# Kernel tuning notes

Measured on AMD Instinct MI355X. Metric: run time of the kernel, lower is better.

Reference implementation:

```python
import jax, jax.numpy as jnp
import numpy as np

N, E, IN, H1, H2 = 100000, 3200000, 128, 64, 64


def setup_inputs() -> dict:
    key = jax.random.key(0)
    ks = jax.random.split(key, 6)
    return {
        "edge_index": jax.random.randint(ks[0], (2, E), 0, N),
        "edge_weight": jax.random.uniform(ks[1], (E,), jnp.float32),
        "emb": jax.random.normal(ks[2], (N, IN), jnp.float32) * 0.05,  # xavier-initialized node embeddings
        "W1": jax.random.normal(ks[3], (IN, H1), jnp.float32) / np.sqrt(IN),
        "b1": jnp.zeros((H1,), jnp.float32),
        "W2": jax.random.normal(ks[4], (H1, H2), jnp.float32) / np.sqrt(H1),
        "b2": jnp.zeros((H2,), jnp.float32),
    }


def _digcn_conv(x, edge_index, edge_weight, W, b):
    # DIGCNConv: dense transform, then weighted sparse neighborhood sum-aggregation.
    x = x @ W                                              # [N, d_out]
    msg = edge_weight[:, None] * x[edge_index[0]]          # gather sources -> [E, d_out]
    out = jax.ops.segment_sum(msg, edge_index[1], num_segments=x.shape[0])  # scatter-add to targets
    return out + b


def reference(edge_index, edge_weight, emb, W1, b1, W2, b2):
    h = jax.nn.relu(_digcn_conv(emb, edge_index, edge_weight, W1, b1))
    # F.dropout with training=False is identity (inference mode)
    return _digcn_conv(h, edge_index, edge_weight, W2, b2)
```

## Files before the change

kernel.cpp:

```cpp
#include <hip/hip_runtime.h>
#include <hip/hip_bf16.h>

#define NNODES 100000
#define DIN 128
#define DH 64
#define SRCMASK 0x1FFFF
#define BSH2 8
#define BN2 256
#define NBUCK2 ((NNODES + BN2 - 1) >> BSH2)
#define NCAP 9088
#define EPB 8192
#define MAXBLK 512
#define OVFCAP 4096

typedef short s16x8 __attribute__((ext_vector_type(8)));
typedef float f32x4 __attribute__((ext_vector_type(4)));

static __device__ __forceinline__ short f2bf(float f) {
  __hip_bfloat16 h = __float2bfloat16(f);
  return *reinterpret_cast<short*>(&h);
}
static __device__ __forceinline__ float bf2f(short s) {
  return __uint_as_float(((unsigned)(unsigned short)s) << 16);
}


__global__ __launch_bounds__(256, 4) void gemm1_mfma(
    const float* __restrict__ emb, const float* __restrict__ W1,
    __hip_bfloat16* __restrict__ x1, int N) {
  __shared__ short Bhi[4 * 4 * 64 * 8];
  __shared__ short Blo[4 * 4 * 64 * 8];
  int tid = threadIdx.x;

  for (int idx = tid; idx < 8192; idx += 256) {
    int i = idx & 7, ln = (idx >> 3) & 63, ct = (idx >> 9) & 3, kc = idx >> 11;
    int k = kc * 32 + (ln >> 4) * 8 + i;
    int col = ct * 16 + (ln & 15);
    float w = W1[k * DH + col];
    short h = f2bf(w);
    Bhi[idx] = h;
    Blo[idx] = f2bf(w - bf2f(h));
  }
  __syncthreads();

  int lane = tid & 63, wv = tid >> 6;
  int r0 = (blockIdx.x * 8 + wv * 2) * 16;
  if (r0 >= N) return;

  const int rA = lane & 15, g = lane >> 4;
  f32x4 acc[2][4] = {};

#pragma unroll
  for (int kc = 0; kc < 4; ++kc) {
    s16x8 ahi[2], alo[2];
#pragma unroll
    for (int rt = 0; rt < 2; ++rt) {
      int r = r0 + rt * 16 + rA;
      float av[8];
      if (r < N) {
        const float4* ap = (const float4*)(emb + (long)r * DIN + kc * 32 + g * 8);
        float4 v0 = ap[0], v1 = ap[1];
        av[0] = v0.x; av[1] = v0.y; av[2] = v0.z; av[3] = v0.w;
        av[4] = v1.x; av[5] = v1.y; av[6] = v1.z; av[7] = v1.w;
      } else {
#pragma unroll
        for (int i = 0; i < 8; ++i) av[i] = 0.f;
      }
#pragma unroll
      for (int i = 0; i < 8; ++i) {
        short h = f2bf(av[i]);
        ahi[rt][i] = h;
        alo[rt][i] = f2bf(av[i] - bf2f(h));
      }
    }
#pragma unroll
    for (int ct = 0; ct < 4; ++ct) {
      int fo = ((kc * 4 + ct) * 64 + lane) * 8;
      s16x8 bh = *(const s16x8*)&Bhi[fo];
      s16x8 bl = *(const s16x8*)&Blo[fo];
#pragma unroll
      for (int rt = 0; rt < 2; ++rt) {
        acc[rt][ct] = __builtin_amdgcn_mfma_f32_16x16x32_bf16(ahi[rt], bh, acc[rt][ct], 0, 0, 0);
        acc[rt][ct] = __builtin_amdgcn_mfma_f32_16x16x32_bf16(alo[rt], bh, acc[rt][ct], 0, 0, 0);
        acc[rt][ct] = __builtin_amdgcn_mfma_f32_16x16x32_bf16(ahi[rt], bl, acc[rt][ct], 0, 0, 0);
      }
    }
  }

#pragma unroll
  for (int rt = 0; rt < 2; ++rt) {
#pragma unroll
    for (int j = 0; j < 4; ++j) {
      int row = r0 + rt * 16 + g * 4 + j;
      if (row < N) {
#pragma unroll
        for (int ct = 0; ct < 4; ++ct)
          x1[(long)row * DH + ct * 16 + rA] = __float2bfloat16(acc[rt][ct][j]);
      }
    }
  }
}

__global__ __launch_bounds__(256, 4) void gemm2_mfma(
    const float* __restrict__ agg, const float* __restrict__ W2,
    const float* __restrict__ b1, __hip_bfloat16* __restrict__ x2, int N) {
  __shared__ short Bhi[2 * 4 * 64 * 8];
  __shared__ short Blo[2 * 4 * 64 * 8];
  int tid = threadIdx.x;

  for (int idx = tid; idx < 4096; idx += 256) {
    int i = idx & 7, ln = (idx >> 3) & 63, ct = (idx >> 9) & 3, kc = (idx >> 11) & 1;
    int k = kc * 32 + (ln >> 4) * 8 + i;
    int col = ct * 16 + (ln & 15);
    float w = W2[k * DH + col];
    short h = f2bf(w);
    Bhi[idx] = h;
    Blo[idx] = f2bf(w - bf2f(h));
  }
  __syncthreads();

  int lane = tid & 63, wv = tid >> 6;
  int r0 = (blockIdx.x * 8 + wv * 2) * 16;
  if (r0 >= N) return;

  const int rA = lane & 15, g = lane >> 4;
  f32x4 acc[2][4] = {};

#pragma unroll
  for (int kc = 0; kc < 2; ++kc) {
    const float4* bp = (const float4*)(b1 + kc * 32 + g * 8);
    float4 b0 = bp[0], b4 = bp[1];
    float bv[8] = {b0.x, b0.y, b0.z, b0.w, b4.x, b4.y, b4.z, b4.w};
    s16x8 ahi[2], alo[2];
#pragma unroll
    for (int rt = 0; rt < 2; ++rt) {
      int r = r0 + rt * 16 + rA;
      float av[8];
      if (r < N) {
        const float4* ap = (const float4*)(agg + (long)r * DH + kc * 32 + g * 8);
        float4 v0 = ap[0], v1 = ap[1];
        av[0] = v0.x; av[1] = v0.y; av[2] = v0.z; av[3] = v0.w;
        av[4] = v1.x; av[5] = v1.y; av[6] = v1.z; av[7] = v1.w;
      } else {
#pragma unroll
        for (int i = 0; i < 8; ++i) av[i] = -1e30f;
      }
#pragma unroll
      for (int i = 0; i < 8; ++i) {
        float a = fmaxf(av[i] + bv[i], 0.f);
        short h = f2bf(a);
        ahi[rt][i] = h;
        alo[rt][i] = f2bf(a - bf2f(h));
      }
    }
#pragma unroll
    for (int ct = 0; ct < 4; ++ct) {
      int fo = ((kc * 4 + ct) * 64 + lane) * 8;
      s16x8 bh = *(const s16x8*)&Bhi[fo];
      s16x8 bl = *(const s16x8*)&Blo[fo];
#pragma unroll
      for (int rt = 0; rt < 2; ++rt) {
        acc[rt][ct] = __builtin_amdgcn_mfma_f32_16x16x32_bf16(ahi[rt], bh, acc[rt][ct], 0, 0, 0);
        acc[rt][ct] = __builtin_amdgcn_mfma_f32_16x16x32_bf16(alo[rt], bh, acc[rt][ct], 0, 0, 0);
        acc[rt][ct] = __builtin_amdgcn_mfma_f32_16x16x32_bf16(ahi[rt], bl, acc[rt][ct], 0, 0, 0);
      }
    }
  }

#pragma unroll
  for (int rt = 0; rt < 2; ++rt) {
#pragma unroll
    for (int j = 0; j < 4; ++j) {
      int row = r0 + rt * 16 + g * 4 + j;
      if (row < N) {
#pragma unroll
        for (int ct = 0; ct < 4; ++ct)
          x2[(long)row * DH + ct * 16 + rA] = __float2bfloat16(acc[rt][ct][j]);
      }
    }
  }
}


__global__ __launch_bounds__(512) void block_sort(
    const int* __restrict__ srcs, const int* __restrict__ dsts,
    const float* __restrict__ w, int2* __restrict__ sorted,
    unsigned short* __restrict__ offTab, int E) {
  __shared__ int2 stage[EPB];
  __shared__ int hist[512];
  __shared__ int sc[512];
  __shared__ int cur[512];
  int tid = threadIdx.x, blk = blockIdx.x;
  int e0 = blk * EPB;

  hist[tid] = 0;
  __syncthreads();

  int pk[16], bd[16];
#pragma unroll
  for (int i = 0; i < 16; ++i) {
    int e = e0 + i * 512 + tid;
    if (e < E) {
      int s = srcs[e], d = dsts[e];
      float wv = w[e];
      int q = (int)(wv * 32768.f + 0.5f);
      if (q > 32767) q = 32767;
      pk[i] = (s & SRCMASK) | (q << 17);
      bd[i] = d;
    } else bd[i] = -1;
  }
#pragma unroll
  for (int i = 0; i < 16; ++i)
    if (bd[i] >= 0) atomicAdd(&hist[bd[i] >> BSH2], 1);
  __syncthreads();

  sc[tid] = (tid < NBUCK2) ? hist[tid] : 0;
  __syncthreads();
  for (int d = 1; d < 512; d <<= 1) {
    int u = (tid >= d) ? sc[tid - d] : 0;
    __syncthreads();
    sc[tid] += u;
    __syncthreads();
  }
  long row = (long)blk * (NBUCK2 + 1);
  if (tid < NBUCK2) {
    int base = sc[tid] - hist[tid];
    cur[tid] = base;
    offTab[row + tid] = (unsigned short)base;
    if (tid == NBUCK2 - 1) offTab[row + NBUCK2] = (unsigned short)sc[tid];
  }
  __syncthreads();

#pragma unroll
  for (int i = 0; i < 16; ++i) {
    if (bd[i] >= 0) {
      int pos = atomicAdd(&cur[bd[i] >> BSH2], 1);
      stage[pos] = make_int2(pk[i], bd[i] & (BN2 - 1));
    }
  }
  __syncthreads();

  int eN = min(EPB, E - e0);
  for (int i = tid; i < eN; i += 512)
    sorted[(long)blk * EPB + i] = stage[i];
}

__global__ __launch_bounds__(512, 2) void sort_gemm1(
    const int* __restrict__ srcs, const int* __restrict__ dsts,
    const float* __restrict__ w, int2* __restrict__ sorted,
    unsigned short* __restrict__ offTab, int E,
    const float* __restrict__ emb, const float* __restrict__ W1,
    __hip_bfloat16* __restrict__ x1, int N, int NBLK, int* __restrict__ ovfcnt) {
  __shared__ __align__(16) char smem[EPB * 8 + 3 * 512 * 4];
  int tid = threadIdx.x;

  if (blockIdx.x >= (unsigned)NBLK) {
    if (blockIdx.x == (unsigned)NBLK && tid == 0) *ovfcnt = 0;
    short* Bhi = (short*)smem;
    short* Blo = Bhi + 8192;
    for (int idx = tid; idx < 8192; idx += 512) {
      int i = idx & 7, ln = (idx >> 3) & 63, ct = (idx >> 9) & 3, kc = idx >> 11;
      int k = kc * 32 + (ln >> 4) * 8 + i;
      int col = ct * 16 + (ln & 15);
      float wv = W1[k * DH + col];
      short h = f2bf(wv);
      Bhi[idx] = h;
      Blo[idx] = f2bf(wv - bf2f(h));
    }
    __syncthreads();

    int lane = tid & 63, wv8 = tid >> 6;
    int gblk = blockIdx.x - NBLK;
    int r0 = gblk * 256 + wv8 * 32;
    if (r0 >= N) return;

    const int rA = lane & 15, g = lane >> 4;
    f32x4 acc[2][4] = {};

#pragma unroll
    for (int kc = 0; kc < 4; ++kc) {
      s16x8 ahi[2], alo[2];
#pragma unroll
      for (int rt = 0; rt < 2; ++rt) {
        int r = r0 + rt * 16 + rA;
        float av[8];
        if (r < N) {
          const float4* ap = (const float4*)(emb + (long)r * DIN + kc * 32 + g * 8);
          float4 v0 = ap[0], v1 = ap[1];
          av[0] = v0.x; av[1] = v0.y; av[2] = v0.z; av[3] = v0.w;
          av[4] = v1.x; av[5] = v1.y; av[6] = v1.z; av[7] = v1.w;
        } else {
#pragma unroll
          for (int i = 0; i < 8; ++i) av[i] = 0.f;
        }
#pragma unroll
        for (int i = 0; i < 8; ++i) {
          short h = f2bf(av[i]);
          ahi[rt][i] = h;
          alo[rt][i] = f2bf(av[i] - bf2f(h));
        }
      }
#pragma unroll
      for (int ct = 0; ct < 4; ++ct) {
        int fo = ((kc * 4 + ct) * 64 + lane) * 8;
        s16x8 bh = *(const s16x8*)&Bhi[fo];
        s16x8 bl = *(const s16x8*)&Blo[fo];
#pragma unroll
        for (int rt = 0; rt < 2; ++rt) {
          acc[rt][ct] = __builtin_amdgcn_mfma_f32_16x16x32_bf16(ahi[rt], bh, acc[rt][ct], 0, 0, 0);
          acc[rt][ct] = __builtin_amdgcn_mfma_f32_16x16x32_bf16(alo[rt], bh, acc[rt][ct], 0, 0, 0);
          acc[rt][ct] = __builtin_amdgcn_mfma_f32_16x16x32_bf16(ahi[rt], bl, acc[rt][ct], 0, 0, 0);
        }
      }
    }

#pragma unroll
    for (int rt = 0; rt < 2; ++rt) {
#pragma unroll
      for (int j = 0; j < 4; ++j) {
        int row = r0 + rt * 16 + g * 4 + j;
        if (row < N) {
#pragma unroll
          for (int ct = 0; ct < 4; ++ct)
            x1[(long)row * DH + ct * 16 + rA] = __float2bfloat16(acc[rt][ct][j]);
        }
      }
    }
    return;
  }

  int2* stage = (int2*)smem;
  int* hist = (int*)(smem + EPB * 8);
  int* sc   = hist + 512;
  int* cur  = sc + 512;
  int blk = blockIdx.x;
  int e0 = blk * EPB;

  hist[tid] = 0;
  __syncthreads();

  int pk[16], bd[16];
#pragma unroll
  for (int i = 0; i < 16; ++i) {
    int e = e0 + i * 512 + tid;
    if (e < E) {
      int s = srcs[e], d = dsts[e];
      float wv = w[e];
      int q = (int)(wv * 32768.f + 0.5f);
      if (q > 32767) q = 32767;
      pk[i] = (s & SRCMASK) | (q << 17);
      bd[i] = d;
    } else bd[i] = -1;
  }
#pragma unroll
  for (int i = 0; i < 16; ++i)
    if (bd[i] >= 0) atomicAdd(&hist[bd[i] >> BSH2], 1);
  __syncthreads();

  sc[tid] = (tid < NBUCK2) ? hist[tid] : 0;
  __syncthreads();
  for (int d = 1; d < 512; d <<= 1) {
    int u = (tid >= d) ? sc[tid - d] : 0;
    __syncthreads();
    sc[tid] += u;
    __syncthreads();
  }
  long row = (long)blk * (NBUCK2 + 1);
  if (tid < NBUCK2) {
    int base = sc[tid] - hist[tid];
    cur[tid] = base;
    offTab[row + tid] = (unsigned short)base;
    if (tid == NBUCK2 - 1) offTab[row + NBUCK2] = (unsigned short)sc[tid];
  }
  __syncthreads();

#pragma unroll
  for (int i = 0; i < 16; ++i) {
    if (bd[i] >= 0) {
      int pos = atomicAdd(&cur[bd[i] >> BSH2], 1);
      stage[pos] = make_int2(pk[i], bd[i] & (BN2 - 1));
    }
  }
  __syncthreads();

  int eN = min(EPB, E - e0);
  for (int i = tid; i < eN; i += 512)
    sorted[(long)blk * EPB + i] = stage[i];
}

__global__ __launch_bounds__(512) void gather_build(
    const unsigned short* __restrict__ offTab, const int2* __restrict__ sorted,
    int* __restrict__ noff, int* __restrict__ ndeg, int* __restrict__ pairs,
    int2* __restrict__ ovf, int* __restrict__ ovfcnt, int NBLK, int N) {
  __shared__ int2 gath[NCAP];
  __shared__ unsigned short offR[MAXBLK];
  __shared__ unsigned short cntR[MAXBLK];
  __shared__ int baseR[MAXBLK];
  __shared__ int sc[512];
  __shared__ int deg[BN2], cur[BN2];
  int b = blockIdx.x, tid = threadIdx.x;

  for (int blk = tid; blk < NBLK; blk += 512) {
    long row = (long)blk * (NBUCK2 + 1);
    int st = offTab[row + b];
    int en = offTab[row + b + 1];
    offR[blk] = (unsigned short)st;
    cntR[blk] = (unsigned short)(en - st);
  }
  __syncthreads();

  sc[tid] = (tid < NBLK) ? (int)cntR[tid] : 0;
  __syncthreads();
  for (int d = 1; d < 512; d <<= 1) {
    int u = (tid >= d) ? sc[tid - d] : 0;
    __syncthreads();
    sc[tid] += u;
    __syncthreads();
  }
  if (tid < NBLK) baseR[tid] = sc[tid] - (int)cntR[tid];
  __syncthreads();
  int total = sc[NBLK - 1];
  int tcl = total > NCAP ? NCAP : total;

  int wv = tid >> 6, lane = tid & 63;
  for (int blk = wv; blk < NBLK; blk += 8) {
    int st = offR[blk], c = cntR[blk], gb = baseR[blk];
    for (int l = lane; l < c; l += 64) {
      int2 v = sorted[(long)blk * EPB + st + l];
      int gp = gb + l;
      if (gp < NCAP) gath[gp] = v;
      else {
        int oi = atomicAdd(ovfcnt, 1);
        if (oi < OVFCAP) ovf[oi] = make_int2(v.x, (b << BSH2) | v.y);
      }
    }
  }
  if (tid < BN2) deg[tid] = 0;
  __syncthreads();

  for (int k = tid; k < tcl; k += 512)
    atomicAdd(&deg[gath[k].y & (BN2 - 1)], 1);
  __syncthreads();

  sc[tid] = (tid < BN2) ? deg[tid] : 0;
  __syncthreads();
  for (int d = 1; d < 512; d <<= 1) {
    int u = (tid >= d) ? sc[tid - d] : 0;
    __syncthreads();
    sc[tid] += u;
    __syncthreads();
  }
  if (tid < BN2) {
    int excl = sc[tid] - deg[tid];
    int gpos = b * NCAP + excl;
    cur[tid] = gpos;
    int n = (b << BSH2) + tid;
    if (n < N) { noff[n] = gpos; ndeg[n] = deg[tid]; }
  }
  __syncthreads();

  for (int k = tid; k < tcl; k += 512) {
    int p = atomicAdd(&cur[gath[k].y & (BN2 - 1)], 1);
    pairs[p] = gath[k].x;
  }
}

__global__ __launch_bounds__(256) void ovf_fixup(
    const int2* __restrict__ ovf, const int* __restrict__ ovfcnt,
    const short* __restrict__ x, float* __restrict__ out) {
  int cnt = *ovfcnt;
  if (cnt > OVFCAP) cnt = OVFCAP;
  int wid = (int)((blockIdx.x * 256 + threadIdx.x) >> 6);
  int lane = threadIdx.x & 63;
  int nw = (gridDim.x * 256) >> 6;
  for (int i = wid; i < cnt; i += nw) {
    int2 e = ovf[i];
    unsigned p = (unsigned)e.x;
    float wv = (float)(p >> 17) * (1.f / 32768.f);
    float xv = bf2f(x[(long)(p & SRCMASK) * DH + lane]);
    atomicAdd(&out[(long)e.y * DH + lane], wv * xv);
  }
}

#define ACC4(P, XV)                                          \
  do {                                                       \
    float wv_ = (float)((P) >> 17) * (1.f / 32768.f);        \
    a0 += wv_ * __uint_as_float((XV).x << 16);               \
    a1 += wv_ * __uint_as_float((XV).x & 0xFFFF0000u);       \
    a2 += wv_ * __uint_as_float((XV).y << 16);               \
    a3 += wv_ * __uint_as_float((XV).y & 0xFFFF0000u);       \
  } while (0)

__global__ __launch_bounds__(256) void agg_quad(
    const int* __restrict__ pairs, const int* __restrict__ noff,
    const int* __restrict__ ndeg,
    const uint2* __restrict__ x,
    const float* __restrict__ bias, float* __restrict__ out, int N) {
  int wid = (int)(((long)blockIdx.x * 256 + threadIdx.x) >> 6);
  int lane = threadIdx.x & 63;
  if (wid >= N) return;
  int h = lane >> 4;
  int fj = lane & 15;
  int st = noff[wid];
  int m = ndeg[wid];
  float a0 = 0.f, a1 = 0.f, a2 = 0.f, a3 = 0.f;

  for (int base = 0; base < m; base += 64) {
    int pl = (base + lane < m) ? pairs[st + base + lane] : 0;
    int mm = m - base;

    unsigned pg[8];
#pragma unroll
    for (int g = 0; g < 8; ++g) pg[g] = (unsigned)__shfl(pl, g * 4 + h);
    uint2 xg[8];
#pragma unroll
    for (int g = 0; g < 8; ++g) xg[g] = x[(pg[g] & SRCMASK) * 16 + fj];
#pragma unroll
    for (int g = 0; g < 8; ++g) ACC4(pg[g], xg[g]);

#pragma unroll
    for (int q = 32; q < 64; q += 16) {
      if (q >= mm) break;
      unsigned p0 = (unsigned)__shfl(pl, q + h);
      unsigned p1 = (unsigned)__shfl(pl, q + 4 + h);
      unsigned p2 = (unsigned)__shfl(pl, q + 8 + h);
      unsigned p3 = (unsigned)__shfl(pl, q + 12 + h);
      uint2 y0 = x[(p0 & SRCMASK) * 16 + fj];
      uint2 y1 = x[(p1 & SRCMASK) * 16 + fj];
      uint2 y2 = x[(p2 & SRCMASK) * 16 + fj];
      uint2 y3 = x[(p3 & SRCMASK) * 16 + fj];
      ACC4(p0, y0); ACC4(p1, y1); ACC4(p2, y2); ACC4(p3, y3);
    }
  }

  a0 += __shfl_xor(a0, 16); a0 += __shfl_xor(a0, 32);
  a1 += __shfl_xor(a1, 16); a1 += __shfl_xor(a1, 32);
  a2 += __shfl_xor(a2, 16); a2 += __shfl_xor(a2, 32);
  a3 += __shfl_xor(a3, 16); a3 += __shfl_xor(a3, 32);
  if (lane < 16) {
    if (bias) {
      float4 bv = ((const float4*)bias)[fj];
      a0 += bv.x; a1 += bv.y; a2 += bv.z; a3 += bv.w;
    }
    ((float4*)out)[(long)wid * 16 + fj] = make_float4(a0, a1, a2, a3);
  }
}


__global__ __launch_bounds__(256) void gemm1_f32(
    const float* __restrict__ emb, const float* __restrict__ W1,
    float* __restrict__ x1, int N) {
  __shared__ float Ws[DIN * DH];
  __shared__ float rows[4][DIN];
  int tid = threadIdx.x;
  for (int i = tid; i < DIN * DH; i += 256) Ws[i] = W1[i];
  int r0 = blockIdx.x * 4;
  for (int i = tid; i < 4 * DIN; i += 256) {
    int rr = i >> 7, kk = i & 127;
    int r = r0 + rr;
    rows[rr][kk] = (r < N) ? emb[(long)r * DIN + kk] : 0.f;
  }
  __syncthreads();
  int rr = tid >> 6, j = tid & 63;
  int r = r0 + rr;
  float acc = 0.f;
#pragma unroll
  for (int k = 0; k < DIN; ++k) acc += rows[rr][k] * Ws[k * DH + j];
  if (r < N) x1[(long)r * DH + j] = acc;
}

__global__ __launch_bounds__(256) void gemm2_f32(
    const float* __restrict__ agg, const float* __restrict__ W2,
    const float* __restrict__ b1, float* __restrict__ x2, int N) {
  __shared__ float Ws[DH * DH];
  __shared__ float rows[4][DH];
  int tid = threadIdx.x;
  for (int i = tid; i < DH * DH; i += 256) Ws[i] = W2[i];
  int r0 = blockIdx.x * 4;
  {
    int rr = tid >> 6, kk = tid & 63;
    int r = r0 + rr;
    float v = (r < N) ? agg[(long)r * DH + kk] + b1[kk] : 0.f;
    rows[rr][kk] = v > 0.f ? v : 0.f;
  }
  __syncthreads();
  int rr = tid >> 6, j = tid & 63;
  float acc = 0.f;
#pragma unroll
  for (int k = 0; k < DH; ++k) acc += rows[rr][k] * Ws[k * DH + j];
  int r = r0 + rr;
  if (r < N) x2[(long)r * DH + j] = acc;
}

__global__ __launch_bounds__(256) void init_bias_kernel(
    float* __restrict__ out, const float* __restrict__ b2, int total) {
  int i = blockIdx.x * 256 + threadIdx.x;
  if (i < total) out[i] = b2[i & 63];
}

__global__ __launch_bounds__(256) void scatter_kernel(
    const int* __restrict__ srcs, const int* __restrict__ dsts,
    const float* __restrict__ w, const float* __restrict__ x,
    float* __restrict__ out, int E) {
  long t = (long)blockIdx.x * 256 + threadIdx.x;
  long e = t >> 6;
  if (e >= E) return;
  int j = (int)(t & 63);
  int s = srcs[e];
  int d = dsts[e];
  float val = w[e] * x[(long)s * DH + j];
  atomicAdd(&out[(long)d * DH + j], val);
}


static inline size_t align256(size_t x) { return (x + 255) & ~(size_t)255; }

extern "C" void kernel_launch(void* const* d_in, const int* in_sizes, int n_in,
                              void* d_out, int out_size, void* d_ws, size_t ws_size,
                              hipStream_t stream) {
  const int*   edge_index = (const int*)d_in[0];
  const float* edge_w     = (const float*)d_in[1];
  const float* emb        = (const float*)d_in[2];
  const float* W1         = (const float*)d_in[3];
  const float* b1         = (const float*)d_in[4];
  const float* W2         = (const float*)d_in[5];
  const float* b2         = (const float*)d_in[6];
  float* out = (float*)d_out;

  const int E = in_sizes[0] / 2;
  const int N = NNODES;
  const int* srcs = edge_index;
  const int* dsts = edge_index + E;

  const int NBLK = (E + EPB - 1) / EPB;

  const size_t sortedbytes = (size_t)NBLK * EPB * sizeof(int2);
  const size_t xbytes_bf   = (size_t)N * DH * sizeof(__hip_bfloat16);
  const size_t offTabbytes = (size_t)NBLK * (NBUCK2 + 1) * sizeof(unsigned short);
  const size_t pairsbytes  = (size_t)NBUCK2 * NCAP * sizeof(int);
  const size_t nbytes      = (size_t)N * sizeof(int);

  const int aggBlocks = (N + 3) / 4;
  const int gemmBlocks = (N + 127) / 128;
  const int g1Blocks   = (N + 255) / 256;

  size_t off = 0;
  char* base = (char*)d_ws;
  int2* sorted = (int2*)(base + off);              off = align256(off + sortedbytes);
  __hip_bfloat16* xbuf = (__hip_bfloat16*)(base + off); off = align256(off + xbytes_bf);
  unsigned short* offTab = (unsigned short*)(base + off); off = align256(off + offTabbytes);
  int* pairs = (int*)(base + off);  off = align256(off + pairsbytes);
  int* noff  = (int*)(base + off);  off = align256(off + nbytes);
  int* ndeg  = (int*)(base + off);  off = align256(off + nbytes);
  int2* ovf  = (int2*)(base + off); off = align256(off + OVFCAP * sizeof(int2));
  int* ovfcnt = (int*)(base + off); off = align256(off + 256);
  const size_t needed_fused = off;

  if (ws_size >= needed_fused && NBLK <= MAXBLK) {
    sort_gemm1<<<NBLK + g1Blocks, 512, 0, stream>>>(
        srcs, dsts, edge_w, sorted, offTab, E, emb, W1, xbuf, N, NBLK, ovfcnt);
    gather_build<<<NBUCK2, 512, 0, stream>>>(offTab, sorted, noff, ndeg, pairs,
                                             ovf, ovfcnt, NBLK, N);
    agg_quad<<<aggBlocks, 256, 0, stream>>>(pairs, noff, ndeg, (const uint2*)xbuf,
                                            nullptr, out, N);
    ovf_fixup<<<8, 256, 0, stream>>>(ovf, ovfcnt, (const short*)xbuf, out);
    gemm2_mfma<<<gemmBlocks, 256, 0, stream>>>(out, W2, b1, xbuf, N);
    agg_quad<<<aggBlocks, 256, 0, stream>>>(pairs, noff, ndeg, (const uint2*)xbuf,
                                            b2, out, N);
    ovf_fixup<<<8, 256, 0, stream>>>(ovf, ovfcnt, (const short*)xbuf, out);
    return;
  }

  off = 0;
  int2* sorted2 = (int2*)(base + off);
  off = align256(off + (sortedbytes > xbytes_bf ? sortedbytes : xbytes_bf));
  __hip_bfloat16* xbuf2 = (__hip_bfloat16*)sorted2;
  unsigned short* offTab2 = (unsigned short*)(base + off); off = align256(off + offTabbytes);
  int* pairs2 = (int*)(base + off);  off = align256(off + pairsbytes);
  int* noff2  = (int*)(base + off);  off = align256(off + nbytes);
  int* ndeg2  = (int*)(base + off);  off = align256(off + nbytes);
  int2* ovf2  = (int2*)(base + off); off = align256(off + OVFCAP * sizeof(int2));
  int* ovfcnt2 = (int*)(base + off); off = align256(off + 256);
  const size_t needed_seq = off;

  if (ws_size >= needed_seq && NBLK <= MAXBLK) {
    hipMemsetAsync(ovfcnt2, 0, sizeof(int), stream);
    block_sort<<<NBLK, 512, 0, stream>>>(srcs, dsts, edge_w, sorted2, offTab2, E);
    gather_build<<<NBUCK2, 512, 0, stream>>>(offTab2, sorted2, noff2, ndeg2, pairs2,
                                             ovf2, ovfcnt2, NBLK, N);
    gemm1_mfma<<<gemmBlocks, 256, 0, stream>>>(emb, W1, xbuf2, N);
    agg_quad<<<aggBlocks, 256, 0, stream>>>(pairs2, noff2, ndeg2, (const uint2*)xbuf2,
                                            nullptr, out, N);
    ovf_fixup<<<8, 256, 0, stream>>>(ovf2, ovfcnt2, (const short*)xbuf2, out);
    gemm2_mfma<<<gemmBlocks, 256, 0, stream>>>(out, W2, b1, xbuf2, N);
    agg_quad<<<aggBlocks, 256, 0, stream>>>(pairs2, noff2, ndeg2, (const uint2*)xbuf2,
                                            b2, out, N);
    ovf_fixup<<<8, 256, 0, stream>>>(ovf2, ovfcnt2, (const short*)xbuf2, out);
    return;
  }

  const long scatterThreads = (long)E * 64;
  const int scatterBlocks = (int)((scatterThreads + 255) / 256);
  const int rowBlocks4 = (N + 3) / 4;
  float* xb1 = (float*)d_ws;

  gemm1_f32<<<rowBlocks4, 256, 0, stream>>>(emb, W1, xb1, N);
  hipMemsetAsync(d_out, 0, (size_t)N * DH * sizeof(float), stream);
  scatter_kernel<<<scatterBlocks, 256, 0, stream>>>(srcs, dsts, edge_w, xb1, out, E);

  gemm2_f32<<<rowBlocks4, 256, 0, stream>>>(out, W2, b1, xb1, N);
  init_bias_kernel<<<(N * DH + 255) / 256, 256, 0, stream>>>(out, b2, N * DH);
  scatter_kernel<<<scatterBlocks, 256, 0, stream>>>(srcs, dsts, edge_w, xb1, out, E);
}
```

Measured before the change: 189.4 us.

## Split sorted edge records into int payload and byte bucket arrays, flatten gather

The intermediate sorted edge buffer is split from 8-byte int2 records into a 4-byte packed source/weight array plus a 1-byte local destination array. This cuts global traffic and shared memory in the sort and gather-build stages, and occupancy hints are raised. gather_build now spreads work evenly over threads, each finding its source sort block by binary search instead of one wave per block. The per-bucket cap is slightly reduced to fit more blocks per CU, which may send more edges down the overflow path. Byte-sized global stores and the per-element binary search add some cost.

```diff
diff --git a/kernel.cpp b/kernel.cpp
--- a/kernel.cpp
+++ b/kernel.cpp
@@ -8,7 +8,7 @@
 #define BSH2 8
 #define BN2 256
 #define NBUCK2 ((NNODES + BN2 - 1) >> BSH2)
-#define NCAP 9088
+#define NCAP 8960
 #define EPB 8192
 #define MAXBLK 512
 #define OVFCAP 4096
@@ -182,11 +182,12 @@
 }
 
 
-__global__ __launch_bounds__(512) void block_sort(
+__global__ __launch_bounds__(512, 6) void block_sort(
     const int* __restrict__ srcs, const int* __restrict__ dsts,
-    const float* __restrict__ w, int2* __restrict__ sorted,
-    unsigned short* __restrict__ offTab, int E) {
-  __shared__ int2 stage[EPB];
+    const float* __restrict__ w, int* __restrict__ spk,
+    unsigned char* __restrict__ sdl, unsigned short* __restrict__ offTab, int E) {
+  __shared__ int stageP[EPB];
+  __shared__ unsigned char stageD[EPB];
   __shared__ int hist[512];
   __shared__ int sc[512];
   __shared__ int cur[512];
@@ -235,23 +236,26 @@
   for (int i = 0; i < 16; ++i) {
     if (bd[i] >= 0) {
       int pos = atomicAdd(&cur[bd[i] >> BSH2], 1);
-      stage[pos] = make_int2(pk[i], bd[i] & (BN2 - 1));
+      stageP[pos] = pk[i];
+      stageD[pos] = (unsigned char)(bd[i] & (BN2 - 1));
     }
   }
   __syncthreads();
 
   int eN = min(EPB, E - e0);
-  for (int i = tid; i < eN; i += 512)
-    sorted[(long)blk * EPB + i] = stage[i];
-}
-
-__global__ __launch_bounds__(512, 2) void sort_gemm1(
+  for (int i = tid; i < eN; i += 512) {
+    spk[(long)blk * EPB + i] = stageP[i];
+    sdl[(long)blk * EPB + i] = stageD[i];
+  }
+}
+
+__global__ __launch_bounds__(512, 6) void sort_gemm1(
     const int* __restrict__ srcs, const int* __restrict__ dsts,
-    const float* __restrict__ w, int2* __restrict__ sorted,
-    unsigned short* __restrict__ offTab, int E,
+    const float* __restrict__ w, int* __restrict__ spk,
+    unsigned char* __restrict__ sdl, unsigned short* __restrict__ offTab, int E,
     const float* __restrict__ emb, const float* __restrict__ W1,
     __hip_bfloat16* __restrict__ x1, int N, int NBLK, int* __restrict__ ovfcnt) {
-  __shared__ __align__(16) char smem[EPB * 8 + 3 * 512 * 4];
+  __shared__ __align__(16) char smem[EPB * 4 + EPB + 3 * 512 * 4];
   int tid = threadIdx.x;
 
   if (blockIdx.x >= (unsigned)NBLK) {
@@ -329,8 +333,9 @@
     return;
   }
 
-  int2* stage = (int2*)smem;
-  int* hist = (int*)(smem + EPB * 8);
+  int* stageP = (int*)smem;
+  unsigned char* stageD = (unsigned char*)(smem + EPB * 4);
+  int* hist = (int*)(smem + EPB * 4 + EPB);
   int* sc   = hist + 512;
   int* cur  = sc + 512;
   int blk = blockIdx.x;
@@ -378,21 +383,26 @@
   for (int i = 0; i < 16; ++i) {
     if (bd[i] >= 0) {
       int pos = atomicAdd(&cur[bd[i] >> BSH2], 1);
-      stage[pos] = make_int2(pk[i], bd[i] & (BN2 - 1));
+      stageP[pos] = pk[i];
+      stageD[pos] = (unsigned char)(bd[i] & (BN2 - 1));
     }
   }
   __syncthreads();
 
   int eN = min(EPB, E - e0);
-  for (int i = tid; i < eN; i += 512)
-    sorted[(long)blk * EPB + i] = stage[i];
-}
-
-__global__ __launch_bounds__(512) void gather_build(
-    const unsigned short* __restrict__ offTab, const int2* __restrict__ sorted,
+  for (int i = tid; i < eN; i += 512) {
+    spk[(long)blk * EPB + i] = stageP[i];
+    sdl[(long)blk * EPB + i] = stageD[i];
+  }
+}
+
+__global__ __launch_bounds__(512, 6) void gather_build(
+    const unsigned short* __restrict__ offTab, const int* __restrict__ spk,
+    const unsigned char* __restrict__ sdl,
     int* __restrict__ noff, int* __restrict__ ndeg, int* __restrict__ pairs,
     int2* __restrict__ ovf, int* __restrict__ ovfcnt, int NBLK, int N) {
-  __shared__ int2 gath[NCAP];
+  __shared__ int gathP[NCAP];
+  __shared__ unsigned char gathD[NCAP];
   __shared__ unsigned short offR[MAXBLK];
   __shared__ unsigned short cntR[MAXBLK];
   __shared__ int baseR[MAXBLK];
@@ -422,24 +432,28 @@
   int total = sc[NBLK - 1];
   int tcl = total > NCAP ? NCAP : total;
 
-  int wv = tid >> 6, lane = tid & 63;
-  for (int blk = wv; blk < NBLK; blk += 8) {
-    int st = offR[blk], c = cntR[blk], gb = baseR[blk];
-    for (int l = lane; l < c; l += 64) {
-      int2 v = sorted[(long)blk * EPB + st + l];
-      int gp = gb + l;
-      if (gp < NCAP) gath[gp] = v;
-      else {
-        int oi = atomicAdd(ovfcnt, 1);
-        if (oi < OVFCAP) ovf[oi] = make_int2(v.x, (b << BSH2) | v.y);
-      }
+  for (int g = tid; g < total; g += 512) {
+    int lo = 0, hi = NBLK - 1;
+    while (lo < hi) {
+      int mid = (lo + hi + 1) >> 1;
+      if (baseR[mid] <= g) lo = mid; else hi = mid - 1;
+    }
+    int pos = (int)offR[lo] + (g - baseR[lo]);
+    int pk = spk[(long)lo * EPB + pos];
+    int dl = sdl[(long)lo * EPB + pos];
+    if (g < NCAP) {
+      gathP[g] = pk;
+      gathD[g] = (unsigned char)dl;
+    } else {
+      int oi = atomicAdd(ovfcnt, 1);
+      if (oi < OVFCAP) ovf[oi] = make_int2(pk, (b << BSH2) | dl);
     }
   }
   if (tid < BN2) deg[tid] = 0;
   __syncthreads();
 
   for (int k = tid; k < tcl; k += 512)
-    atomicAdd(&deg[gath[k].y & (BN2 - 1)], 1);
+    atomicAdd(&deg[gathD[k]], 1);
   __syncthreads();
 
   sc[tid] = (tid < BN2) ? deg[tid] : 0;
@@ -460,8 +474,8 @@
   __syncthreads();
 
   for (int k = tid; k < tcl; k += 512) {
-    int p = atomicAdd(&cur[gath[k].y & (BN2 - 1)], 1);
-    pairs[p] = gath[k].x;
+    int p = atomicAdd(&cur[gathD[k]], 1);
+    pairs[p] = gathP[k];
   }
 }
 
@@ -634,7 +648,8 @@
 
   const int NBLK = (E + EPB - 1) / EPB;
 
-  const size_t sortedbytes = (size_t)NBLK * EPB * sizeof(int2);
+  const size_t spkbytes    = (size_t)NBLK * EPB * sizeof(int);
+  const size_t sdlbytes    = (size_t)NBLK * EPB;
   const size_t xbytes_bf   = (size_t)N * DH * sizeof(__hip_bfloat16);
   const size_t offTabbytes = (size_t)NBLK * (NBUCK2 + 1) * sizeof(unsigned short);
   const size_t pairsbytes  = (size_t)NBUCK2 * NCAP * sizeof(int);
@@ -646,7 +661,8 @@
 
   size_t off = 0;
   char* base = (char*)d_ws;
-  int2* sorted = (int2*)(base + off);              off = align256(off + sortedbytes);
+  int* spk = (int*)(base + off);                   off = align256(off + spkbytes);
+  unsigned char* sdl = (unsigned char*)(base + off); off = align256(off + sdlbytes);
   __hip_bfloat16* xbuf = (__hip_bfloat16*)(base + off); off = align256(off + xbytes_bf);
   unsigned short* offTab = (unsigned short*)(base + off); off = align256(off + offTabbytes);
   int* pairs = (int*)(base + off);  off = align256(off + pairsbytes);
@@ -658,8 +674,8 @@
 
   if (ws_size >= needed_fused && NBLK <= MAXBLK) {
     sort_gemm1<<<NBLK + g1Blocks, 512, 0, stream>>>(
-        srcs, dsts, edge_w, sorted, offTab, E, emb, W1, xbuf, N, NBLK, ovfcnt);
-    gather_build<<<NBUCK2, 512, 0, stream>>>(offTab, sorted, noff, ndeg, pairs,
+        srcs, dsts, edge_w, spk, sdl, offTab, E, emb, W1, xbuf, N, NBLK, ovfcnt);
+    gather_build<<<NBUCK2, 512, 0, stream>>>(offTab, spk, sdl, noff, ndeg, pairs,
                                              ovf, ovfcnt, NBLK, N);
     agg_quad<<<aggBlocks, 256, 0, stream>>>(pairs, noff, ndeg, (const uint2*)xbuf,
                                             nullptr, out, N);
@@ -672,9 +688,10 @@
   }
 
   off = 0;
-  int2* sorted2 = (int2*)(base + off);
-  off = align256(off + (sortedbytes > xbytes_bf ? sortedbytes : xbytes_bf));
-  __hip_bfloat16* xbuf2 = (__hip_bfloat16*)sorted2;
+  int* spk2 = (int*)(base + off);
+  off = align256(off + (spkbytes > xbytes_bf ? spkbytes : xbytes_bf));
+  __hip_bfloat16* xbuf2 = (__hip_bfloat16*)spk2;
+  unsigned char* sdl2 = (unsigned char*)(base + off); off = align256(off + sdlbytes);
   unsigned short* offTab2 = (unsigned short*)(base + off); off = align256(off + offTabbytes);
   int* pairs2 = (int*)(base + off);  off = align256(off + pairsbytes);
   int* noff2  = (int*)(base + off);  off = align256(off + nbytes);
@@ -685,8 +702,8 @@
 
   if (ws_size >= needed_seq && NBLK <= MAXBLK) {
     hipMemsetAsync(ovfcnt2, 0, sizeof(int), stream);
-    block_sort<<<NBLK, 512, 0, stream>>>(srcs, dsts, edge_w, sorted2, offTab2, E);
-    gather_build<<<NBUCK2, 512, 0, stream>>>(offTab2, sorted2, noff2, ndeg2, pairs2,
+    block_sort<<<NBLK, 512, 0, stream>>>(srcs, dsts, edge_w, spk2, sdl2, offTab2, E);
+    gather_build<<<NBUCK2, 512, 0, stream>>>(offTab2, spk2, sdl2, noff2, ndeg2, pairs2,
                                              ovf2, ovfcnt2, NBLK, N);
     gemm1_mfma<<<gemmBlocks, 256, 0, stream>>>(emb, W1, xbuf2, N);
     agg_quad<<<aggBlocks, 256, 0, stream>>>(pairs2, noff2, ndeg2, (const uint2*)xbuf2,
```

Result: faster. 182.0 us (-3.9%).
